# Optimization experiments

Measured on AMD Instinct MI355X. Metric: run time of the kernel, lower is better.

## Reference

```python
import jax, jax.numpy as jnp
import numpy as np

N = 50000        # nodes
E = 800000       # edges (avg degree 16)
D = 128          # input_dim
H = 128          # hidden_channels
OUT = 1          # output_dim
NUM_GRAPHS = 512 # graphs in batch (fixed for jit; == batch.max()+1)


def setup_inputs() -> dict:
    key = jax.random.key(0)
    ks = jax.random.split(key, 12)
    x = jax.random.normal(ks[0], (N, D), dtype=jnp.float32)
    edge_index = jax.random.randint(ks[1], (2, E), 0, N, dtype=jnp.int64)
    batch = jnp.sort(jax.random.randint(ks[2], (N,), 0, NUM_GRAPHS, dtype=jnp.int64))
    init = lambda k, shape, fan: jax.random.normal(k, shape, jnp.float32) * np.float32(1.0 / np.sqrt(fan))
    W1 = init(ks[3], (D, H), D); b1 = jnp.zeros((H,), jnp.float32)
    W2 = init(ks[4], (H, H), H); b2 = jnp.zeros((H,), jnp.float32)
    W3 = init(ks[5], (H, H), H); b3 = jnp.zeros((H,), jnp.float32)
    Wo = init(ks[6], (H, OUT), H); bo = jnp.zeros((OUT,), jnp.float32)
    return {"x": x, "edge_index": edge_index, "batch": batch,
            "W1": W1, "b1": b1, "W2": W2, "b2": b2, "W3": W3, "b3": b3,
            "Wo": Wo, "bo": bo}


def _gcn_layer(h, W, b, src, dst, dinv_sqrt):
    # GCNConv: x' = D^{-1/2}(A+I)D^{-1/2} X W + b  (self-loops added)
    hw = h @ W                                        # [N, H]
    coef = (dinv_sqrt[src] * dinv_sqrt[dst])[:, None] # [E, 1]
    agg = jax.ops.segment_sum(hw[src] * coef, dst, num_segments=N)
    agg = agg + hw * (dinv_sqrt * dinv_sqrt)[:, None] # self-loop term: deg^{-1}
    return agg + b


def reference(x, edge_index, batch, W1, b1, W2, b2, W3, b3, Wo, bo):
    src, dst = edge_index[0], edge_index[1]
    # degree from A+I (PyG computes deg on the target/col index)
    deg = jax.ops.segment_sum(jnp.ones((E,), x.dtype), dst, num_segments=N) + 1.0
    dinv_sqrt = jax.lax.rsqrt(deg)
    h = jax.nn.relu(_gcn_layer(x, W1, b1, src, dst, dinv_sqrt))
    h = jax.nn.relu(_gcn_layer(h, W2, b2, src, dst, dinv_sqrt))
    h = _gcn_layer(h, W3, b3, src, dst, dinv_sqrt)   # last conv: no relu
    pooled = jax.ops.segment_sum(h, batch, num_segments=NUM_GRAPHS)  # global_add_pool
    # F.dropout(p=0.1) is identity in eval mode
    return pooled @ Wo + bo                           # [NUM_GRAPHS, 1]
```

## Files before the change

kernel.cpp:

```cpp
#include <hip/hip_runtime.h>

typedef _Float16 f16;
typedef unsigned short u16;
typedef __attribute__((ext_vector_type(2))) _Float16 f16x2;
typedef __attribute__((ext_vector_type(8))) _Float16 f16x8;
typedef __attribute__((ext_vector_type(8))) unsigned short u16x8;
typedef __attribute__((ext_vector_type(4))) float f32x4;
typedef __attribute__((ext_vector_type(4))) int intx4;

#define STRIDE 64
#define SLAB   5120

__device__ inline float2 h2f(unsigned u){
    f16x2 h = __builtin_bit_cast(f16x2, u);
    return make_float2((float)h.x, (float)h.y);
}

__device__ inline void addrow(float* acc, uint4 u){
    float2 p0 = h2f(u.x), p1 = h2f(u.y), p2 = h2f(u.z), p3 = h2f(u.w);
    acc[0] += p0.x; acc[1] += p0.y; acc[2] += p1.x; acc[3] += p1.y;
    acc[4] += p2.x; acc[5] += p2.y; acc[6] += p3.x; acc[7] += p3.y;
}


__global__ __launch_bounds__(256) void k_bucket(const int* __restrict__ src, const int* __restrict__ dst,
                                                int* __restrict__ bucketCnt, unsigned* __restrict__ bucketBuf,
                                                int NB, int E4, int E){
    __shared__ int hist[256], pos[256];
    int t = threadIdx.x;
    hist[t] = 0;
    __syncthreads();
    int i4a = blockIdx.x*512 + t;
    int i4b = i4a + 256;
    bool va = i4a < E4, vb = i4b < E4;
    intx4 da = {}, db = {}, sa = {}, sb = {};
    if (va){ da = __builtin_nontemporal_load((const intx4*)dst + i4a);
             sa = __builtin_nontemporal_load((const intx4*)src + i4a); }
    if (vb){ db = __builtin_nontemporal_load((const intx4*)dst + i4b);
             sb = __builtin_nontemporal_load((const intx4*)src + i4b); }
    auto cnt1 = [&](int e, int d){ if (e < E) atomicAdd(&hist[d >> 8], 1); };
    if (va){ int b0 = i4a*4; cnt1(b0,da.x); cnt1(b0+1,da.y); cnt1(b0+2,da.z); cnt1(b0+3,da.w); }
    if (vb){ int b0 = i4b*4; cnt1(b0,db.x); cnt1(b0+1,db.y); cnt1(b0+2,db.z); cnt1(b0+3,db.w); }
    __syncthreads();
    if (t < NB && hist[t] > 0) pos[t] = atomicAdd(&bucketCnt[t], hist[t]);
    __syncthreads();
    auto put1 = [&](int e, int d, int s){
        if (e < E){
            int b = d >> 8;
            int slot = atomicAdd(&pos[b], 1);
            if (slot < SLAB)
                bucketBuf[(size_t)b*SLAB + slot] = ((unsigned)(d & 255) << 16) | (unsigned)s;
        }
    };
    if (va){ int b0 = i4a*4; put1(b0,da.x,sa.x); put1(b0+1,da.y,sa.y); put1(b0+2,da.z,sa.z); put1(b0+3,da.w,sa.w); }
    if (vb){ int b0 = i4b*4; put1(b0,db.x,sb.x); put1(b0+1,db.y,sb.y); put1(b0+2,db.z,sb.z); put1(b0+3,db.w,sb.w); }
}


__global__ __launch_bounds__(256) void k_build(const unsigned* __restrict__ bucketBuf,
                                               const int* __restrict__ bucketCnt,
                                               u16* __restrict__ csr, int* __restrict__ fil,
                                               float* __restrict__ dinv, int* __restrict__ blkh, int N){
    __shared__ u16 rows[256*64];
    __shared__ int cnt[256];
    __shared__ int h8[8];
    int t = threadIdx.x;
    cnt[t] = 0;
    if (t < 8) h8[t] = 0;
    u16x8 fillv;
    #pragma unroll
    for (int j = 0; j < 8; ++j) fillv[j] = (u16)N;
    #pragma unroll
    for (int j = 0; j < 8; ++j) *(u16x8*)&rows[t*64 + j*8] = fillv;
    __syncthreads();
    int b = blockIdx.x;
    int cb = min(bucketCnt[b], SLAB);
    for (int e = t; e < cb; e += 256){
        unsigned v = bucketBuf[(size_t)b*SLAB + e];
        int off = v >> 16;
        int p = atomicAdd(&cnt[off], 1);
        if (p < STRIDE){
            int ch = ((p >> 3) ^ (off & 7));
            rows[off*64 + ch*8 + (p & 7)] = (u16)(v & 0xffff);
        }
    }
    __syncthreads();
    int node = b*256 + t;
    if (node <= N){
        int c = cnt[t];
        fil[node] = c;
        dinv[node] = rsqrtf((float)c + 1.0f);
        if (node < N){
            int nb = (min(c, STRIDE) + 7) >> 3;
            if (nb > 7) nb = 7;
            atomicAdd(&h8[nb], 1);
        }
        u16x8* d8 = (u16x8*)&csr[(size_t)node*64];
        #pragma unroll
        for (int j = 0; j < 8; ++j)
            d8[j] = *(u16x8*)&rows[t*64 + ((j ^ (t & 7))*8)];
    }
    __syncthreads();
    if (t < 8) blkh[b*8 + t] = h8[t];
}

__global__ __launch_bounds__(256) void k_bscan(const int* __restrict__ blkh, int* __restrict__ blkoff,
                                               int* __restrict__ ord, uint4* __restrict__ hwrows,
                                               int N, int NQ4, int nbB){
    __shared__ int sm[8][256];
    int t = threadIdx.x;
    int v[8];
    #pragma unroll
    for (int b = 0; b < 8; ++b){
        v[b] = (t < nbB) ? blkh[t*8 + b] : 0;
        sm[b][t] = v[b];
    }
    __syncthreads();
    for (int off = 1; off < 256; off <<= 1){
        int u[8];
        #pragma unroll
        for (int b = 0; b < 8; ++b) u[b] = (t >= off) ? sm[b][t-off] : 0;
        __syncthreads();
        #pragma unroll
        for (int b = 0; b < 8; ++b) sm[b][t] += u[b];
        __syncthreads();
    }
    int s = 0;
    int bases[8];
    #pragma unroll
    for (int b = 0; b < 8; ++b){ bases[b] = s; s += sm[b][255]; }
    if (t < nbB){
        #pragma unroll
        for (int b = 0; b < 8; ++b)
            blkoff[t*8 + b] = sm[b][t] - v[b] + bases[b];
    }
    if (t >= 200 && t < 216) hwrows[(size_t)N*16 + (t - 200)] = make_uint4(0,0,0,0);
    for (int i = N + t; i < NQ4; i += 256) ord[i] = N;
}

__global__ __launch_bounds__(256) void k_scatterL(const int* __restrict__ fil, const int* __restrict__ blkoff,
                                                  int* __restrict__ ord, int N){
    __shared__ int off[8];
    int t = threadIdx.x;
    if (t < 8) off[t] = blkoff[blockIdx.x*8 + t];
    __syncthreads();
    int i = blockIdx.x*256 + t;
    if (i < N){
        int nb = (min(fil[i], STRIDE) + 7) >> 3;
        if (nb > 7) nb = 7;
        int p = atomicAdd(&off[nb], 1);
        ord[p] = i;
    }
}


__global__ __launch_bounds__(128) void k_prep(const float* __restrict__ W3, const float* __restrict__ Wo,
                                              const float* __restrict__ b3, float* __restrict__ u,
                                              float* __restrict__ su, float* __restrict__ zs,
                                              float* __restrict__ out, const float* __restrict__ bo,
                                              int N, int G){
    __shared__ float sWo[128];
    __shared__ float red[128];
    int t = threadIdx.x;
    sWo[t] = Wo[t];
    __syncthreads();
    float s = 0.f;
    for (int c2 = 0; c2 < 128; ++c2) s = fmaf(W3[t*128 + c2], sWo[c2], s);
    u[t] = s;
    red[t] = b3[t] * sWo[t];
    __syncthreads();
    for (int o = 64; o > 0; o >>= 1){
        if (t < o) red[t] += red[t+o];
        __syncthreads();
    }
    if (t == 0){ *su = red[0]; zs[N] = 0.f; }
    float bv = bo[0];
    for (int g2 = t; g2 < G; g2 += 128) out[g2] = bv;
}


#define LDW 136

template<int AFP16>
__global__ __launch_bounds__(256) void k_mm(const void* __restrict__ Av, const float* __restrict__ W,
                                            const float* __restrict__ dinv, f16* __restrict__ C, int n){
    __shared__ __align__(16) _Float16 sWt[128*LDW];
    __shared__ __align__(16) _Float16 sOut[4][16*LDW];
    int t = threadIdx.x;
    for (int idx = t; idx < 4096; idx += 256){
        int k = idx >> 5, c4 = (idx & 31) * 4;
        float4 w = ((const float4*)W)[idx];
        sWt[(c4+0)*LDW + k] = (f16)w.x;
        sWt[(c4+1)*LDW + k] = (f16)w.y;
        sWt[(c4+2)*LDW + k] = (f16)w.z;
        sWt[(c4+3)*LDW + k] = (f16)w.w;
    }
    __syncthreads();

    int wv = t >> 6, l = t & 63;
    int r16 = l & 15, g = l >> 4;
    int r0 = blockIdx.x * 64 + wv * 16;

    int arow = r0 + r16;
    bool aok = arow < n;
    f16x8 a[4];
    #pragma unroll
    for (int s = 0; s < 4; ++s){
        if (AFP16){
            const f16* A = (const f16*)Av;
            a[s] = aok ? *(const f16x8*)&A[(size_t)arow*128 + s*32 + g*8] : (f16x8)(_Float16)0.f;
        } else {
            const float* A = (const float*)Av;
            f16x8 av = (f16x8)(_Float16)0.f;
            if (aok){
                const float4* ap = (const float4*)&A[(size_t)arow*128 + s*32 + g*8];
                float4 x0 = ap[0], x1 = ap[1];
                av[0]=(f16)x0.x; av[1]=(f16)x0.y; av[2]=(f16)x0.z; av[3]=(f16)x0.w;
                av[4]=(f16)x1.x; av[5]=(f16)x1.y; av[6]=(f16)x1.z; av[7]=(f16)x1.w;
            }
            a[s] = av;
        }
    }

    f32x4 acc[8];
    #pragma unroll
    for (int ct = 0; ct < 8; ++ct) acc[ct] = (f32x4)0.f;

    #pragma unroll
    for (int ct = 0; ct < 8; ++ct){
        int c = ct*16 + r16;
        #pragma unroll
        for (int s = 0; s < 4; ++s){
            f16x8 b = *(const f16x8*)&sWt[c*LDW + s*32 + g*8];
            acc[ct] = __builtin_amdgcn_mfma_f32_16x16x32_f16(a[s], b, acc[ct], 0, 0, 0);
        }
    }

    float dv[4];
    #pragma unroll
    for (int j = 0; j < 4; ++j){
        int rr = r0 + g*4 + j;
        dv[j] = (rr < n) ? dinv[rr] : 0.f;
    }
    #pragma unroll
    for (int ct = 0; ct < 8; ++ct)
        #pragma unroll
        for (int j = 0; j < 4; ++j)
            sOut[wv][(g*4+j)*LDW + ct*16 + r16] = (f16)(acc[ct][j] * dv[j]);
    __syncthreads();

    int orow = r0 + r16;
    if (orow < n){
        const f16x8* srcp = (const f16x8*)&sOut[wv][r16*LDW + g*32];
        f16x8 o0 = srcp[0], o1 = srcp[1], o2 = srcp[2], o3 = srcp[3];
        f16x8* dstp = (f16x8*)&C[(size_t)orow*128 + g*32];
        dstp[0]=o0; dstp[1]=o1; dstp[2]=o2; dstp[3]=o3;
    }
}


#define AGG_BODY \
    int l = threadIdx.x & 63; \
    int g = l >> 4, c = l & 15; \
    intx4 wq = *((const intx4*)ord + wvi); \
    int w0 = __builtin_amdgcn_readfirstlane(wq.x); \
    int w1 = __builtin_amdgcn_readfirstlane(wq.y); \
    int w2 = __builtin_amdgcn_readfirstlane(wq.z); \
    int w3 = __builtin_amdgcn_readfirstlane(wq.w); \
    int wsel = (g==0) ? w0 : (g==1) ? w1 : (g==2) ? w2 : w3; \
    const uint4* rows = (const uint4*)hw; \
    float acc[8] = {0,0,0,0,0,0,0,0}; \
    { uint4 s = rows[(size_t)wsel*16 + c]; addrow(acc, s); } \
    int nb0=(min(fil[w0],STRIDE)+7)>>3, nb1=(min(fil[w1],STRIDE)+7)>>3; \
    int nb2=(min(fil[w2],STRIDE)+7)>>3, nb3=(min(fil[w3],STRIDE)+7)>>3; \
    int nbm  = max(max(nb0,nb1), max(nb2,nb3)); \
    int nbsel = (g==0) ? nb0 : (g==1) ? nb1 : (g==2) ? nb2 : nb3; \
    const u16* cp = csr + (size_t)wsel*STRIDE; \
    for (int t2 = 0; t2 < nbm; ++t2){ \
        if (t2 < nbsel){ \
            u16x8 iv = *(const u16x8*)cp; cp += 8; \
            uint4 r0 = rows[(size_t)iv[0]*16 + c]; \
            uint4 r1 = rows[(size_t)iv[1]*16 + c]; \
            uint4 r2 = rows[(size_t)iv[2]*16 + c]; \
            uint4 r3 = rows[(size_t)iv[3]*16 + c]; \
            uint4 r4 = rows[(size_t)iv[4]*16 + c]; \
            uint4 r5 = rows[(size_t)iv[5]*16 + c]; \
            uint4 r6 = rows[(size_t)iv[6]*16 + c]; \
            uint4 r7 = rows[(size_t)iv[7]*16 + c]; \
            addrow(acc, r0); addrow(acc, r1); addrow(acc, r2); addrow(acc, r3); \
            addrow(acc, r4); addrow(acc, r5); addrow(acc, r6); addrow(acc, r7); \
        } \
    }

__global__ __launch_bounds__(256) void k_agg4(const f16* __restrict__ hw, const float* __restrict__ dinv,
                                              const int* __restrict__ fil, const u16* __restrict__ csr,
                                              const int* __restrict__ ord, const float* __restrict__ bias,
                                              f16* __restrict__ hout, int N, int NQ){
    int wvi = (blockIdx.x*256 + threadIdx.x) >> 6;
    if (wvi >= NQ) return;
    AGG_BODY
    if (wsel < N){
        float di = dinv[wsel];
        const float4* bp = (const float4*)bias + c*2;
        float4 b0 = bp[0], b1 = bp[1];
        f16x8 o;
        o[0]=(f16)fmaxf(fmaf(acc[0],di,b0.x),0.f); o[1]=(f16)fmaxf(fmaf(acc[1],di,b0.y),0.f);
        o[2]=(f16)fmaxf(fmaf(acc[2],di,b0.z),0.f); o[3]=(f16)fmaxf(fmaf(acc[3],di,b0.w),0.f);
        o[4]=(f16)fmaxf(fmaf(acc[4],di,b1.x),0.f); o[5]=(f16)fmaxf(fmaf(acc[5],di,b1.y),0.f);
        o[6]=(f16)fmaxf(fmaf(acc[6],di,b1.z),0.f); o[7]=(f16)fmaxf(fmaf(acc[7],di,b1.w),0.f);
        *(f16x8*)&hout[(size_t)wsel*128 + c*8] = o;
    }
}

__global__ __launch_bounds__(256) void k_agg4z(const f16* __restrict__ hw, const float* __restrict__ dinv,
                                               const int* __restrict__ fil, const u16* __restrict__ csr,
                                               const int* __restrict__ ord, const float* __restrict__ bias,
                                               const float* __restrict__ u, float* __restrict__ zs,
                                               int N, int NQ){
    int wvi = (blockIdx.x*256 + threadIdx.x) >> 6;
    if (wvi >= NQ) return;
    AGG_BODY
    float di = dinv[wsel];
    const float4* bp = (const float4*)bias + c*2;
    const float4* up = (const float4*)u    + c*2;
    float4 b0 = bp[0], b1 = bp[1];
    float4 u0 = up[0], u1 = up[1];
    float dot = fmaxf(fmaf(acc[0],di,b0.x),0.f)*u0.x + fmaxf(fmaf(acc[1],di,b0.y),0.f)*u0.y
              + fmaxf(fmaf(acc[2],di,b0.z),0.f)*u0.z + fmaxf(fmaf(acc[3],di,b0.w),0.f)*u0.w
              + fmaxf(fmaf(acc[4],di,b1.x),0.f)*u1.x + fmaxf(fmaf(acc[5],di,b1.y),0.f)*u1.y
              + fmaxf(fmaf(acc[6],di,b1.z),0.f)*u1.z + fmaxf(fmaf(acc[7],di,b1.w),0.f)*u1.w;
    dot += __shfl_xor(dot, 1);
    dot += __shfl_xor(dot, 2);
    dot += __shfl_xor(dot, 4);
    dot += __shfl_xor(dot, 8);
    if (c == 0 && wsel < N) zs[wsel] = di * dot;
}


__global__ __launch_bounds__(256) void k_aggs(const float* __restrict__ zs, const float* __restrict__ dinv,
                                              const int* __restrict__ fil, const u16* __restrict__ csr,
                                              const int* __restrict__ batch, const float* __restrict__ supt,
                                              float* __restrict__ out, int N){
    __shared__ float bins[512];
    int t = threadIdx.x;
    bins[t] = 0.f; bins[t+256] = 0.f;
    __syncthreads();
    int i = blockIdx.x*256 + t;
    if (i < N){
        float acc = zs[i];
        int nb = (min(fil[i], STRIDE) + 7) >> 3;
        const u16* cp = csr + (size_t)i*STRIDE;
        for (int b = 0; b < nb; ++b){
            u16x8 iv = *(const u16x8*)cp; cp += 8;
            float s0 = zs[iv[0]] + zs[iv[1]], s1 = zs[iv[2]] + zs[iv[3]];
            float s2 = zs[iv[4]] + zs[iv[5]], s3 = zs[iv[6]] + zs[iv[7]];
            acc += (s0 + s1) + (s2 + s3);
        }
        float tv = fmaf(dinv[i], acc, *supt);
        atomicAdd(&bins[batch[i]], tv);
    }
    __syncthreads();
    float v0 = bins[t], v1 = bins[t+256];
    if (v0 != 0.f) atomicAdd(&out[t], v0);
    if (v1 != 0.f) atomicAdd(&out[t+256], v1);
}


extern "C" void kernel_launch(void* const* d_in, const int* in_sizes, int n_in,
                              void* d_out, int out_size, void* d_ws, size_t ws_size,
                              hipStream_t stream) {
    const float* x     = (const float*)d_in[0];
    const int*   ei    = (const int*)d_in[1];
    const int*   batch = (const int*)d_in[2];
    const float* W1 = (const float*)d_in[3];
    const float* b1 = (const float*)d_in[4];
    const float* W2 = (const float*)d_in[5];
    const float* b2 = (const float*)d_in[6];
    const float* W3 = (const float*)d_in[7];
    const float* b3 = (const float*)d_in[8];
    const float* Wo = (const float*)d_in[9];
    const float* bo = (const float*)d_in[10];

    int N = in_sizes[0] / 128;
    int E = in_sizes[1] / 2;
    int G = out_size;
    const int* srcI = ei;
    const int* dstI = ei + E;

    int NQ  = (N + 3) / 4;
    int NQ4 = NQ * 4;
    int NB  = (N + 256) / 256;
    int E4  = (E + 3) / 4;
    int nbK = (E + 2047) / 2048;

    char* p = (char*)d_ws;
    size_t off = 0;
    auto alloc = [&](size_t bytes) -> void* {
        void* r = p + off;
        off += (bytes + 255) & ~(size_t)255;
        return r;
    };
    f16*      hw      = (f16*)alloc((size_t)(N+1)*128*sizeof(f16));
    f16*      h       = (f16*)alloc((size_t)N*128*sizeof(f16));
    float*    dinv    = (float*)alloc((size_t)(N+1)*sizeof(float));
    int*      fil     = (int*)alloc((size_t)(N+1)*sizeof(int));
    int*      blkh    = (int*)alloc((size_t)NB*8*sizeof(int));
    int*      blkoff  = (int*)alloc((size_t)NB*8*sizeof(int));
    int*      ord     = (int*)alloc((size_t)NQ4*sizeof(int));
    float*    zs      = (float*)alloc((size_t)(N+1)*sizeof(float));
    float*    uvec    = (float*)alloc(128*sizeof(float));
    float*    su      = (float*)alloc(sizeof(float));
    int*      bucketCnt = (int*)alloc((size_t)NB*sizeof(int));
    unsigned* bucketBuf = (unsigned*)alloc((size_t)NB*SLAB*sizeof(unsigned));
    u16*      csr     = (u16*)alloc((size_t)(N+1)*STRIDE*sizeof(u16));

    hipMemsetAsync(bucketCnt, 0, (size_t)NB*sizeof(int), stream);

    k_bucket  <<<nbK, 256, 0, stream>>>(srcI, dstI, bucketCnt, bucketBuf, NB, E4, E);
    k_build   <<<NB,  256, 0, stream>>>(bucketBuf, bucketCnt, csr, fil, dinv, blkh, N);
    k_bscan   <<<1,   256, 0, stream>>>(blkh, blkoff, ord, (uint4*)hw, N, NQ4, NB);
    k_scatterL<<<NB,  256, 0, stream>>>(fil, blkoff, ord, N);
    k_prep    <<<1,   128, 0, stream>>>(W3, Wo, b3, uvec, su, zs, (float*)d_out, bo, N, G);

    int nbM = (N + 63)/64;
    int nbA = (int)(((size_t)NQ*64 + 255)/256);

    k_mm<0> <<<nbM, 256, 0, stream>>>(x, W1, dinv, hw, N);
    k_agg4  <<<nbA, 256, 0, stream>>>(hw, dinv, fil, csr, ord, b1, h, N, NQ);
    k_mm<1> <<<nbM, 256, 0, stream>>>(h, W2, dinv, hw, N);
    k_agg4z <<<nbA, 256, 0, stream>>>(hw, dinv, fil, csr, ord, b2, uvec, zs, N, NQ);
    k_aggs  <<<NB,  256, 0, stream>>>(zs, dinv, fil, csr, batch, su, (float*)d_out, N);
}
```

Measured before the change: 161.6 us.

## Merge setup launches, fuse degree scatter with first GEMM, refine degree buckets

Drops the memset by zeroing bucket counters inside k_prep, which now launches first. The degree-bucket scatter and the first dense transform run as one launch, with blocks split by index and sharing a shared-memory union. Degree bucketing moves from granularity 8 to 4 across 16 buckets, so the aggregation loops walk 4-neighbour chunks and waste fewer padded gathers per wave. The cost is more loop iterations with fewer loads in flight per iteration, plus a larger scan.

```diff
diff --git a/kernel.cpp b/kernel.cpp
--- a/kernel.cpp
+++ b/kernel.cpp
@@ -4,12 +4,15 @@
 typedef unsigned short u16;
 typedef __attribute__((ext_vector_type(2))) _Float16 f16x2;
 typedef __attribute__((ext_vector_type(8))) _Float16 f16x8;
+typedef __attribute__((ext_vector_type(4))) unsigned short u16x4;
 typedef __attribute__((ext_vector_type(8))) unsigned short u16x8;
 typedef __attribute__((ext_vector_type(4))) float f32x4;
 typedef __attribute__((ext_vector_type(4))) int intx4;
 
 #define STRIDE 64
 #define SLAB   5120
+#define LDW    136
+#define NBUK   16
 
 __device__ inline float2 h2f(unsigned u){
     f16x2 h = __builtin_bit_cast(f16x2, u);
@@ -22,170 +25,38 @@
     acc[4] += p2.x; acc[5] += p2.y; acc[6] += p3.x; acc[7] += p3.y;
 }
 
-
-__global__ __launch_bounds__(256) void k_bucket(const int* __restrict__ src, const int* __restrict__ dst,
-                                                int* __restrict__ bucketCnt, unsigned* __restrict__ bucketBuf,
-                                                int NB, int E4, int E){
-    __shared__ int hist[256], pos[256];
-    int t = threadIdx.x;
-    hist[t] = 0;
-    __syncthreads();
-    int i4a = blockIdx.x*512 + t;
-    int i4b = i4a + 256;
-    bool va = i4a < E4, vb = i4b < E4;
-    intx4 da = {}, db = {}, sa = {}, sb = {};
-    if (va){ da = __builtin_nontemporal_load((const intx4*)dst + i4a);
-             sa = __builtin_nontemporal_load((const intx4*)src + i4a); }
-    if (vb){ db = __builtin_nontemporal_load((const intx4*)dst + i4b);
-             sb = __builtin_nontemporal_load((const intx4*)src + i4b); }
-    auto cnt1 = [&](int e, int d){ if (e < E) atomicAdd(&hist[d >> 8], 1); };
-    if (va){ int b0 = i4a*4; cnt1(b0,da.x); cnt1(b0+1,da.y); cnt1(b0+2,da.z); cnt1(b0+3,da.w); }
-    if (vb){ int b0 = i4b*4; cnt1(b0,db.x); cnt1(b0+1,db.y); cnt1(b0+2,db.z); cnt1(b0+3,db.w); }
-    __syncthreads();
-    if (t < NB && hist[t] > 0) pos[t] = atomicAdd(&bucketCnt[t], hist[t]);
-    __syncthreads();
-    auto put1 = [&](int e, int d, int s){
-        if (e < E){
-            int b = d >> 8;
-            int slot = atomicAdd(&pos[b], 1);
-            if (slot < SLAB)
-                bucketBuf[(size_t)b*SLAB + slot] = ((unsigned)(d & 255) << 16) | (unsigned)s;
-        }
-    };
-    if (va){ int b0 = i4a*4; put1(b0,da.x,sa.x); put1(b0+1,da.y,sa.y); put1(b0+2,da.z,sa.z); put1(b0+3,da.w,sa.w); }
-    if (vb){ int b0 = i4b*4; put1(b0,db.x,sb.x); put1(b0+1,db.y,sb.y); put1(b0+2,db.z,sb.z); put1(b0+3,db.w,sb.w); }
-}
-
-
-__global__ __launch_bounds__(256) void k_build(const unsigned* __restrict__ bucketBuf,
-                                               const int* __restrict__ bucketCnt,
-                                               u16* __restrict__ csr, int* __restrict__ fil,
-                                               float* __restrict__ dinv, int* __restrict__ blkh, int N){
-    __shared__ u16 rows[256*64];
-    __shared__ int cnt[256];
-    __shared__ int h8[8];
-    int t = threadIdx.x;
-    cnt[t] = 0;
-    if (t < 8) h8[t] = 0;
-    u16x8 fillv;
-    #pragma unroll
-    for (int j = 0; j < 8; ++j) fillv[j] = (u16)N;
-    #pragma unroll
-    for (int j = 0; j < 8; ++j) *(u16x8*)&rows[t*64 + j*8] = fillv;
-    __syncthreads();
-    int b = blockIdx.x;
-    int cb = min(bucketCnt[b], SLAB);
-    for (int e = t; e < cb; e += 256){
-        unsigned v = bucketBuf[(size_t)b*SLAB + e];
-        int off = v >> 16;
-        int p = atomicAdd(&cnt[off], 1);
-        if (p < STRIDE){
-            int ch = ((p >> 3) ^ (off & 7));
-            rows[off*64 + ch*8 + (p & 7)] = (u16)(v & 0xffff);
-        }
-    }
-    __syncthreads();
-    int node = b*256 + t;
-    if (node <= N){
-        int c = cnt[t];
-        fil[node] = c;
-        dinv[node] = rsqrtf((float)c + 1.0f);
-        if (node < N){
-            int nb = (min(c, STRIDE) + 7) >> 3;
-            if (nb > 7) nb = 7;
-            atomicAdd(&h8[nb], 1);
-        }
-        u16x8* d8 = (u16x8*)&csr[(size_t)node*64];
-        #pragma unroll
-        for (int j = 0; j < 8; ++j)
-            d8[j] = *(u16x8*)&rows[t*64 + ((j ^ (t & 7))*8)];
-    }
-    __syncthreads();
-    if (t < 8) blkh[b*8 + t] = h8[t];
-}
-
-__global__ __launch_bounds__(256) void k_bscan(const int* __restrict__ blkh, int* __restrict__ blkoff,
-                                               int* __restrict__ ord, uint4* __restrict__ hwrows,
-                                               int N, int NQ4, int nbB){
-    __shared__ int sm[8][256];
-    int t = threadIdx.x;
-    int v[8];
-    #pragma unroll
-    for (int b = 0; b < 8; ++b){
-        v[b] = (t < nbB) ? blkh[t*8 + b] : 0;
-        sm[b][t] = v[b];
-    }
-    __syncthreads();
-    for (int off = 1; off < 256; off <<= 1){
-        int u[8];
-        #pragma unroll
-        for (int b = 0; b < 8; ++b) u[b] = (t >= off) ? sm[b][t-off] : 0;
-        __syncthreads();
-        #pragma unroll
-        for (int b = 0; b < 8; ++b) sm[b][t] += u[b];
-        __syncthreads();
-    }
-    int s = 0;
-    int bases[8];
-    #pragma unroll
-    for (int b = 0; b < 8; ++b){ bases[b] = s; s += sm[b][255]; }
-    if (t < nbB){
-        #pragma unroll
-        for (int b = 0; b < 8; ++b)
-            blkoff[t*8 + b] = sm[b][t] - v[b] + bases[b];
-    }
-    if (t >= 200 && t < 216) hwrows[(size_t)N*16 + (t - 200)] = make_uint4(0,0,0,0);
-    for (int i = N + t; i < NQ4; i += 256) ord[i] = N;
-}
-
-__global__ __launch_bounds__(256) void k_scatterL(const int* __restrict__ fil, const int* __restrict__ blkoff,
-                                                  int* __restrict__ ord, int N){
-    __shared__ int off[8];
-    int t = threadIdx.x;
-    if (t < 8) off[t] = blkoff[blockIdx.x*8 + t];
-    __syncthreads();
-    int i = blockIdx.x*256 + t;
-    if (i < N){
-        int nb = (min(fil[i], STRIDE) + 7) >> 3;
-        if (nb > 7) nb = 7;
-        int p = atomicAdd(&off[nb], 1);
-        ord[p] = i;
-    }
-}
-
-
-__global__ __launch_bounds__(128) void k_prep(const float* __restrict__ W3, const float* __restrict__ Wo,
-                                              const float* __restrict__ b3, float* __restrict__ u,
-                                              float* __restrict__ su, float* __restrict__ zs,
-                                              float* __restrict__ out, const float* __restrict__ bo,
-                                              int N, int G){
-    __shared__ float sWo[128];
-    __shared__ float red[128];
-    int t = threadIdx.x;
-    sWo[t] = Wo[t];
-    __syncthreads();
-    float s = 0.f;
-    for (int c2 = 0; c2 < 128; ++c2) s = fmaf(W3[t*128 + c2], sWo[c2], s);
-    u[t] = s;
-    red[t] = b3[t] * sWo[t];
-    __syncthreads();
-    for (int o = 64; o > 0; o >>= 1){
-        if (t < o) red[t] += red[t+o];
-        __syncthreads();
-    }
-    if (t == 0){ *su = red[0]; zs[N] = 0.f; }
-    float bv = bo[0];
-    for (int g2 = t; g2 < G; g2 += 128) out[g2] = bv;
-}
-
-
-#define LDW 136
+#define AGG_BODY \
+    int l = threadIdx.x & 63; \
+    int g = l >> 4, c = l & 15; \
+    intx4 wq = *((const intx4*)ord + wvi); \
+    int w0 = __builtin_amdgcn_readfirstlane(wq.x); \
+    int w1 = __builtin_amdgcn_readfirstlane(wq.y); \
+    int w2 = __builtin_amdgcn_readfirstlane(wq.z); \
+    int w3 = __builtin_amdgcn_readfirstlane(wq.w); \
+    int wsel = (g==0) ? w0 : (g==1) ? w1 : (g==2) ? w2 : w3; \
+    const uint4* rows = (const uint4*)hw; \
+    float acc[8] = {0,0,0,0,0,0,0,0}; \
+    { uint4 s = rows[(size_t)wsel*16 + c]; addrow(acc, s); } \
+    int nb0=(min(fil[w0],STRIDE)+3)>>2, nb1=(min(fil[w1],STRIDE)+3)>>2; \
+    int nb2=(min(fil[w2],STRIDE)+3)>>2, nb3=(min(fil[w3],STRIDE)+3)>>2; \
+    int nbm  = max(max(nb0,nb1), max(nb2,nb3)); \
+    int nbsel = (g==0) ? nb0 : (g==1) ? nb1 : (g==2) ? nb2 : nb3; \
+    const u16* cp = csr + (size_t)wsel*STRIDE; \
+    for (int t2 = 0; t2 < nbm; ++t2){ \
+        if (t2 < nbsel){ \
+            u16x4 iv = *(const u16x4*)cp; cp += 4; \
+            uint4 r0 = rows[(size_t)iv[0]*16 + c]; \
+            uint4 r1 = rows[(size_t)iv[1]*16 + c]; \
+            uint4 r2 = rows[(size_t)iv[2]*16 + c]; \
+            uint4 r3 = rows[(size_t)iv[3]*16 + c]; \
+            addrow(acc, r0); addrow(acc, r1); addrow(acc, r2); addrow(acc, r3); \
+        } \
+    }
 
 template<int AFP16>
-__global__ __launch_bounds__(256) void k_mm(const void* __restrict__ Av, const float* __restrict__ W,
-                                            const float* __restrict__ dinv, f16* __restrict__ C, int n){
-    __shared__ __align__(16) _Float16 sWt[128*LDW];
-    __shared__ __align__(16) _Float16 sOut[4][16*LDW];
+__device__ __forceinline__ void mm_dev(const void* Av, const float* W, const float* dinv,
+                                       f16* C, int n, int vb,
+                                       _Float16* sWt, _Float16 (*sOut)[16*LDW]){
     int t = threadIdx.x;
     for (int idx = t; idx < 4096; idx += 256){
         int k = idx >> 5, c4 = (idx & 31) * 4;
@@ -199,7 +70,7 @@
 
     int wv = t >> 6, l = t & 63;
     int r16 = l & 15, g = l >> 4;
-    int r0 = blockIdx.x * 64 + wv * 16;
+    int r0 = vb * 64 + wv * 16;
 
     int arow = r0 + r16;
     bool aok = arow < n;
@@ -225,7 +96,6 @@
     f32x4 acc[8];
     #pragma unroll
     for (int ct = 0; ct < 8; ++ct) acc[ct] = (f32x4)0.f;
-
     #pragma unroll
     for (int ct = 0; ct < 8; ++ct){
         int c = ct*16 + r16;
@@ -251,46 +121,190 @@
 
     int orow = r0 + r16;
     if (orow < n){
-        const f16x8* srcp = (const f16x8*)&sOut[wv][r16*LDW + g*32];
-        f16x8 o0 = srcp[0], o1 = srcp[1], o2 = srcp[2], o3 = srcp[3];
-        f16x8* dstp = (f16x8*)&C[(size_t)orow*128 + g*32];
-        dstp[0]=o0; dstp[1]=o1; dstp[2]=o2; dstp[3]=o3;
-    }
-}
-
-
-#define AGG_BODY \
-    int l = threadIdx.x & 63; \
-    int g = l >> 4, c = l & 15; \
-    intx4 wq = *((const intx4*)ord + wvi); \
-    int w0 = __builtin_amdgcn_readfirstlane(wq.x); \
-    int w1 = __builtin_amdgcn_readfirstlane(wq.y); \
-    int w2 = __builtin_amdgcn_readfirstlane(wq.z); \
-    int w3 = __builtin_amdgcn_readfirstlane(wq.w); \
-    int wsel = (g==0) ? w0 : (g==1) ? w1 : (g==2) ? w2 : w3; \
-    const uint4* rows = (const uint4*)hw; \
-    float acc[8] = {0,0,0,0,0,0,0,0}; \
-    { uint4 s = rows[(size_t)wsel*16 + c]; addrow(acc, s); } \
-    int nb0=(min(fil[w0],STRIDE)+7)>>3, nb1=(min(fil[w1],STRIDE)+7)>>3; \
-    int nb2=(min(fil[w2],STRIDE)+7)>>3, nb3=(min(fil[w3],STRIDE)+7)>>3; \
-    int nbm  = max(max(nb0,nb1), max(nb2,nb3)); \
-    int nbsel = (g==0) ? nb0 : (g==1) ? nb1 : (g==2) ? nb2 : nb3; \
-    const u16* cp = csr + (size_t)wsel*STRIDE; \
-    for (int t2 = 0; t2 < nbm; ++t2){ \
-        if (t2 < nbsel){ \
-            u16x8 iv = *(const u16x8*)cp; cp += 8; \
-            uint4 r0 = rows[(size_t)iv[0]*16 + c]; \
-            uint4 r1 = rows[(size_t)iv[1]*16 + c]; \
-            uint4 r2 = rows[(size_t)iv[2]*16 + c]; \
-            uint4 r3 = rows[(size_t)iv[3]*16 + c]; \
-            uint4 r4 = rows[(size_t)iv[4]*16 + c]; \
-            uint4 r5 = rows[(size_t)iv[5]*16 + c]; \
-            uint4 r6 = rows[(size_t)iv[6]*16 + c]; \
-            uint4 r7 = rows[(size_t)iv[7]*16 + c]; \
-            addrow(acc, r0); addrow(acc, r1); addrow(acc, r2); addrow(acc, r3); \
-            addrow(acc, r4); addrow(acc, r5); addrow(acc, r6); addrow(acc, r7); \
-        } \
-    }
+        const f16x8* sp = (const f16x8*)&sOut[wv][r16*LDW + g*32];
+        f16x8 o0 = sp[0], o1 = sp[1], o2 = sp[2], o3 = sp[3];
+        f16x8* dp = (f16x8*)&C[(size_t)orow*128 + g*32];
+        dp[0]=o0; dp[1]=o1; dp[2]=o2; dp[3]=o3;
+    }
+}
+
+
+__global__ __launch_bounds__(128) void k_prep(const float* __restrict__ W3, const float* __restrict__ Wo,
+                                              const float* __restrict__ b3, float* __restrict__ u,
+                                              float* __restrict__ su, float* __restrict__ zs,
+                                              float* __restrict__ out, const float* __restrict__ bo,
+                                              int* __restrict__ bucketCnt, int NB, int N, int G){
+    __shared__ float sWo[128];
+    __shared__ float red[128];
+    int t = threadIdx.x;
+    sWo[t] = Wo[t];
+    for (int i = t; i < NB; i += 128) bucketCnt[i] = 0;
+    __syncthreads();
+    float s = 0.f;
+    for (int c2 = 0; c2 < 128; ++c2) s = fmaf(W3[t*128 + c2], sWo[c2], s);
+    u[t] = s;
+    red[t] = b3[t] * sWo[t];
+    __syncthreads();
+    for (int o = 64; o > 0; o >>= 1){
+        if (t < o) red[t] += red[t+o];
+        __syncthreads();
+    }
+    if (t == 0){ *su = red[0]; zs[N] = 0.f; }
+    float bv = bo[0];
+    for (int g2 = t; g2 < G; g2 += 128) out[g2] = bv;
+}
+
+
+__global__ __launch_bounds__(256) void k_bucket(const int* __restrict__ src, const int* __restrict__ dst,
+                                                int* __restrict__ bucketCnt, unsigned* __restrict__ bucketBuf,
+                                                int NB, int E4, int E){
+    __shared__ int hist[256], pos[256];
+    int t = threadIdx.x;
+    hist[t] = 0;
+    __syncthreads();
+    int i4a = blockIdx.x*512 + t;
+    int i4b = i4a + 256;
+    bool va = i4a < E4, vb = i4b < E4;
+    intx4 da = {}, db = {}, sa = {}, sb = {};
+    if (va){ da = __builtin_nontemporal_load((const intx4*)dst + i4a);
+             sa = __builtin_nontemporal_load((const intx4*)src + i4a); }
+    if (vb){ db = __builtin_nontemporal_load((const intx4*)dst + i4b);
+             sb = __builtin_nontemporal_load((const intx4*)src + i4b); }
+    auto cnt1 = [&](int e, int d){ if (e < E) atomicAdd(&hist[d >> 8], 1); };
+    if (va){ int b0 = i4a*4; cnt1(b0,da.x); cnt1(b0+1,da.y); cnt1(b0+2,da.z); cnt1(b0+3,da.w); }
+    if (vb){ int b0 = i4b*4; cnt1(b0,db.x); cnt1(b0+1,db.y); cnt1(b0+2,db.z); cnt1(b0+3,db.w); }
+    __syncthreads();
+    if (t < NB && hist[t] > 0) pos[t] = atomicAdd(&bucketCnt[t], hist[t]);
+    __syncthreads();
+    auto put1 = [&](int e, int d, int s){
+        if (e < E){
+            int b = d >> 8;
+            int slot = atomicAdd(&pos[b], 1);
+            if (slot < SLAB)
+                bucketBuf[(size_t)b*SLAB + slot] = ((unsigned)(d & 255) << 16) | (unsigned)s;
+        }
+    };
+    if (va){ int b0 = i4a*4; put1(b0,da.x,sa.x); put1(b0+1,da.y,sa.y); put1(b0+2,da.z,sa.z); put1(b0+3,da.w,sa.w); }
+    if (vb){ int b0 = i4b*4; put1(b0,db.x,sb.x); put1(b0+1,db.y,sb.y); put1(b0+2,db.z,sb.z); put1(b0+3,db.w,sb.w); }
+}
+
+
+__global__ __launch_bounds__(256) void k_build(const unsigned* __restrict__ bucketBuf,
+                                               const int* __restrict__ bucketCnt,
+                                               u16* __restrict__ csr, int* __restrict__ fil,
+                                               float* __restrict__ dinv, int* __restrict__ blkh, int N){
+    __shared__ u16 rows[256*64];
+    __shared__ int cnt[256];
+    __shared__ int h16[NBUK];
+    int t = threadIdx.x;
+    cnt[t] = 0;
+    if (t < NBUK) h16[t] = 0;
+    u16x8 fillv;
+    #pragma unroll
+    for (int j = 0; j < 8; ++j) fillv[j] = (u16)N;
+    #pragma unroll
+    for (int j = 0; j < 8; ++j) *(u16x8*)&rows[t*64 + j*8] = fillv;
+    __syncthreads();
+    int b = blockIdx.x;
+    int cb = min(bucketCnt[b], SLAB);
+    for (int e = t; e < cb; e += 256){
+        unsigned v = bucketBuf[(size_t)b*SLAB + e];
+        int off = v >> 16;
+        int p = atomicAdd(&cnt[off], 1);
+        if (p < STRIDE){
+            int ch = ((p >> 3) ^ (off & 7));
+            rows[off*64 + ch*8 + (p & 7)] = (u16)(v & 0xffff);
+        }
+    }
+    __syncthreads();
+    int node = b*256 + t;
+    if (node <= N){
+        int c = cnt[t];
+        fil[node] = c;
+        dinv[node] = rsqrtf((float)c + 1.0f);
+        if (node < N){
+            int nb = (min(c, STRIDE) + 3) >> 2;
+            if (nb > NBUK-1) nb = NBUK-1;
+            atomicAdd(&h16[nb], 1);
+        }
+        u16x8* d8 = (u16x8*)&csr[(size_t)node*64];
+        #pragma unroll
+        for (int j = 0; j < 8; ++j)
+            d8[j] = *(u16x8*)&rows[t*64 + ((j ^ (t & 7))*8)];
+    }
+    __syncthreads();
+    if (t < NBUK) blkh[b*NBUK + t] = h16[t];
+}
+
+
+__global__ __launch_bounds__(256) void k_bscan(const int* __restrict__ blkh, int* __restrict__ blkoff,
+                                               int* __restrict__ ord, uint4* __restrict__ hwrows,
+                                               int N, int NQ4, int nbB){
+    __shared__ int sm[NBUK][256];
+    int t = threadIdx.x;
+    int v[NBUK];
+    #pragma unroll
+    for (int b = 0; b < NBUK; ++b){
+        v[b] = (t < nbB) ? blkh[t*NBUK + b] : 0;
+        sm[b][t] = v[b];
+    }
+    __syncthreads();
+    for (int off = 1; off < 256; off <<= 1){
+        int u[NBUK];
+        #pragma unroll
+        for (int b = 0; b < NBUK; ++b) u[b] = (t >= off) ? sm[b][t-off] : 0;
+        __syncthreads();
+        #pragma unroll
+        for (int b = 0; b < NBUK; ++b) sm[b][t] += u[b];
+        __syncthreads();
+    }
+    int s = 0;
+    int bases[NBUK];
+    #pragma unroll
+    for (int b = 0; b < NBUK; ++b){ bases[b] = s; s += sm[b][255]; }
+    if (t < nbB){
+        #pragma unroll
+        for (int b = 0; b < NBUK; ++b)
+            blkoff[t*NBUK + b] = sm[b][t] - v[b] + bases[b];
+    }
+    if (t >= 200 && t < 216) hwrows[(size_t)N*16 + (t - 200)] = make_uint4(0,0,0,0);
+    for (int i = N + t; i < NQ4; i += 256) ord[i] = N;
+}
+
+
+__global__ __launch_bounds__(256) void k_scmm1(const int* __restrict__ fil, const int* __restrict__ blkoff,
+                                               int* __restrict__ ord,
+                                               const float* __restrict__ x, const float* __restrict__ W1,
+                                               const float* __restrict__ dinv, f16* __restrict__ hw,
+                                               int N, int NB){
+    __shared__ __align__(16) union {
+        int off[NBUK];
+        struct { _Float16 sWt[128*LDW]; _Float16 sOut[4][16*LDW]; } mm;
+    } S;
+    int t = threadIdx.x;
+    int vb = blockIdx.x;
+    if (vb < NB){
+        if (t < NBUK) S.off[t] = blkoff[vb*NBUK + t];
+        __syncthreads();
+        int i = vb*256 + t;
+        if (i < N){
+            int nb = (min(fil[i], STRIDE) + 3) >> 2;
+            if (nb > NBUK-1) nb = NBUK-1;
+            int p = atomicAdd(&S.off[nb], 1);
+            ord[p] = i;
+        }
+    } else {
+        mm_dev<0>(x, W1, dinv, hw, N, vb - NB, S.mm.sWt, S.mm.sOut);
+    }
+}
+
+__global__ __launch_bounds__(256) void k_mm2(const f16* __restrict__ A, const float* __restrict__ W,
+                                             const float* __restrict__ dinv, f16* __restrict__ C, int n){
+    __shared__ __align__(16) _Float16 sWt[128*LDW];
+    __shared__ __align__(16) _Float16 sOut[4][16*LDW];
+    mm_dev<1>(A, W, dinv, C, n, blockIdx.x, sWt, sOut);
+}
+
 
 __global__ __launch_bounds__(256) void k_agg4(const f16* __restrict__ hw, const float* __restrict__ dinv,
                                               const int* __restrict__ fil, const u16* __restrict__ csr,
@@ -336,7 +350,6 @@
     if (c == 0 && wsel < N) zs[wsel] = di * dot;
 }
 
-
 __global__ __launch_bounds__(256) void k_aggs(const float* __restrict__ zs, const float* __restrict__ dinv,
                                               const int* __restrict__ fil, const u16* __restrict__ csr,
                                               const int* __restrict__ batch, const float* __restrict__ supt,
@@ -348,13 +361,13 @@
     int i = blockIdx.x*256 + t;
     if (i < N){
         float acc = zs[i];
-        int nb = (min(fil[i], STRIDE) + 7) >> 3;
+        int nb = (min(fil[i], STRIDE) + 3) >> 2;
         const u16* cp = csr + (size_t)i*STRIDE;
         for (int b = 0; b < nb; ++b){
-            u16x8 iv = *(const u16x8*)cp; cp += 8;
-            float s0 = zs[iv[0]] + zs[iv[1]], s1 = zs[iv[2]] + zs[iv[3]];
-            float s2 = zs[iv[4]] + zs[iv[5]], s3 = zs[iv[6]] + zs[iv[7]];
-            acc += (s0 + s1) + (s2 + s3);
+            u16x4 iv = *(const u16x4*)cp; cp += 4;
+            float s0 = zs[iv[0]] + zs[iv[1]];
+            float s1 = zs[iv[2]] + zs[iv[3]];
+            acc += s0 + s1;
         }
         float tv = fmaf(dinv[i], acc, *supt);
         atomicAdd(&bins[batch[i]], tv);
@@ -392,6 +405,7 @@
     int NB  = (N + 256) / 256;
     int E4  = (E + 3) / 4;
     int nbK = (E + 2047) / 2048;
+    int nbM = (N + 63) / 64;
 
     char* p = (char*)d_ws;
     size_t off = 0;
@@ -404,30 +418,25 @@
     f16*      h       = (f16*)alloc((size_t)N*128*sizeof(f16));
     float*    dinv    = (float*)alloc((size_t)(N+1)*sizeof(float));
     int*      fil     = (int*)alloc((size_t)(N+1)*sizeof(int));
-    int*      blkh    = (int*)alloc((size_t)NB*8*sizeof(int));
-    int*      blkoff  = (int*)alloc((size_t)NB*8*sizeof(int));
+    int*      blkh    = (int*)alloc((size_t)NB*NBUK*sizeof(int));
+    int*      blkoff  = (int*)alloc((size_t)NB*NBUK*sizeof(int));
     int*      ord     = (int*)alloc((size_t)NQ4*sizeof(int));
     float*    zs      = (float*)alloc((size_t)(N+1)*sizeof(float));
     float*    uvec    = (float*)alloc(128*sizeof(float));
-    float*    su      = (float*)alloc(sizeof(float));
+    float*    su      = (float*)alloc(256);
     int*      bucketCnt = (int*)alloc((size_t)NB*sizeof(int));
     unsigned* bucketBuf = (unsigned*)alloc((size_t)NB*SLAB*sizeof(unsigned));
     u16*      csr     = (u16*)alloc((size_t)(N+1)*STRIDE*sizeof(u16));
 
-    hipMemsetAsync(bucketCnt, 0, (size_t)NB*sizeof(int), stream);
-
-    k_bucket  <<<nbK, 256, 0, stream>>>(srcI, dstI, bucketCnt, bucketBuf, NB, E4, E);
-    k_build   <<<NB,  256, 0, stream>>>(bucketBuf, bucketCnt, csr, fil, dinv, blkh, N);
-    k_bscan   <<<1,   256, 0, stream>>>(blkh, blkoff, ord, (uint4*)hw, N, NQ4, NB);
-    k_scatterL<<<NB,  256, 0, stream>>>(fil, blkoff, ord, N);
-    k_prep    <<<1,   128, 0, stream>>>(W3, Wo, b3, uvec, su, zs, (float*)d_out, bo, N, G);
-
-    int nbM = (N + 63)/64;
+    k_prep   <<<1,       128, 0, stream>>>(W3, Wo, b3, uvec, su, zs, (float*)d_out, bo, bucketCnt, NB, N, G);
+    k_bucket <<<nbK,     256, 0, stream>>>(srcI, dstI, bucketCnt, bucketBuf, NB, E4, E);
+    k_build  <<<NB,      256, 0, stream>>>(bucketBuf, bucketCnt, csr, fil, dinv, blkh, N);
+    k_bscan  <<<1,       256, 0, stream>>>(blkh, blkoff, ord, (uint4*)hw, N, NQ4, NB);
+    k_scmm1  <<<NB+nbM,  256, 0, stream>>>(fil, blkoff, ord, x, W1, dinv, hw, N, NB);
+
     int nbA = (int)(((size_t)NQ*64 + 255)/256);
-
-    k_mm<0> <<<nbM, 256, 0, stream>>>(x, W1, dinv, hw, N);
     k_agg4  <<<nbA, 256, 0, stream>>>(hw, dinv, fil, csr, ord, b1, h, N, NQ);
-    k_mm<1> <<<nbM, 256, 0, stream>>>(h, W2, dinv, hw, N);
+    k_mm2   <<<nbM, 256, 0, stream>>>(h, W2, dinv, hw, N);
     k_agg4z <<<nbA, 256, 0, stream>>>(hw, dinv, fil, csr, ord, b2, uvec, zs, N, NQ);
     k_aggs  <<<NB,  256, 0, stream>>>(zs, dinv, fil, csr, batch, su, (float*)d_out, N);
 }
```

Result: faster. 157.4 us (-2.6%).
